# Optimization experiments

Hardware: AMD Instinct MI355X
Metric: run time of the kernel (lower is better)

The kernel has to match this reference:

```python
import jax, jax.numpy as jnp
import numpy as np

B, L, C, R, DK = 8, 2048, 512, 64, 64
H = 2 * C  # hdnSize
NEG = -32767.0  # -2**15 + 1
EPS = 1e-5


def _p(key, shape, std=0.02):
    return (jax.random.normal(key, shape, dtype=jnp.float32) * std)


def setup_inputs() -> dict:
    key = jax.random.key(0)
    ks = jax.random.split(key, 16)
    inp = {
        "x": jax.random.normal(ks[0], (B, L, C), dtype=jnp.float32),
        "maskPAD": jax.random.randint(ks[1], (B, 1, L), 0, 2, dtype=jnp.int32),
        "preScores": jax.random.normal(ks[2], (B, R, R), dtype=jnp.float32),
        "Wp": _p(ks[3], (C, R)), "bp": jnp.zeros((R,), jnp.float32),
        "Wq": _p(ks[4], (C, DK)), "bq": jnp.zeros((DK,), jnp.float32),
        "Wk": _p(ks[5], (C, DK)), "bk": jnp.zeros((DK,), jnp.float32),
        "Wv": _p(ks[6], (C, H)), "bv": jnp.zeros((H,), jnp.float32),
        "Wu": _p(ks[7], (C, H)), "bu": jnp.zeros((H,), jnp.float32),
        "Wo": _p(ks[8], (H, C)), "bo": jnp.zeros((C,), jnp.float32),
        "gamma": jnp.ones((C,), jnp.float32),
        "beta": jnp.zeros((C,), jnp.float32),
    }
    return inp


def reference(x, maskPAD, preScores, Wp, bp, Wq, bq, Wk, bk, Wv, bv, Wu, bu, Wo, bo, gamma, beta):
    # GLU gate: [B,L,H]
    gate = jax.nn.silu(x @ Wu + bu)
    # pseudo-attention logits [B,L,r], masked on padded positions
    pScore = x @ Wp + bp
    pad = (maskPAD[:, 0] == 0)[..., None]  # [B,L,1]
    pScore = jnp.where(pad, NEG, pScore)
    pAlpha = jax.nn.softmax(pScore, axis=1)    # softmax over L (dim=-2)
    pAlpha_ = jax.nn.softmax(pScore, axis=-1)  # softmax over r
    # compress: px [B,r,C]  (== pAlpha.transpose(-1,-2) @ x)
    px = jnp.einsum('blr,blc->brc', pAlpha, x)
    q = jax.nn.silu(px @ Wq + bq)  # [B,r,dk]
    k = jax.nn.silu(px @ Wk + bk)  # [B,r,dk]
    v = jax.nn.silu(px @ Wv + bv)  # [B,r,H]
    scores = jnp.einsum('brd,bsd->brs', q, k) / np.sqrt(DK).astype(np.float32)
    scores = scores + preScores
    alpha = jax.nn.softmax(scores, axis=2)
    z = alpha @ v                                # [B,r,H]
    z = jnp.einsum('blr,brh->blh', pAlpha_, z)   # expand back to [B,L,H]
    z = gate * z
    z = z @ Wo + bo                              # [B,L,C]
    y = x + z
    mu = jnp.mean(y, axis=-1, keepdims=True)
    var = jnp.var(y, axis=-1, keepdims=True)
    out = (y - mu) * jax.lax.rsqrt(var + EPS) * gamma + beta
    return out
```

## Files before the change

### kernel.cpp

```cpp
#include <hip/hip_runtime.h>
#include <hip/hip_bf16.h>

constexpr int B_ = 8;
constexpr int L_ = 2048;
constexpr int C_ = 512;
constexpr int R_ = 64;
constexpr int DK_ = 64;
constexpr int H_ = 1024;
constexpr int M_ = B_ * L_;
constexpr int NQKV_ = 1152;
constexpr float NEG_ = -32767.0f;

__device__ __forceinline__ float toF(float x) { return x; }
__device__ __forceinline__ float toF(__hip_bfloat16 x) { return __bfloat162float(x); }
__device__ __forceinline__ float siluf(float v) { return v / (1.0f + __expf(-v)); }
__device__ __forceinline__ ushort bfbits(float f) {
    __hip_bfloat16 h = __float2bfloat16(f);
    union { __hip_bfloat16 h; ushort u; } cv; cv.h = h; return cv.u;
}
__device__ __forceinline__ float bf2f(ushort u) {
    union { uint u; float f; } cv; cv.u = (uint)u << 16; return cv.f;
}

typedef __attribute__((ext_vector_type(8))) short bf16x8;
// ... 40 lines not shown
    int br1 = n0 + s1 * 16 + sr; if (br1 >= Ndim) br1 = Ndim - 1;
    const ushort* a0p = A  + (size_t)(m0 + s0 * 16 + sr) * Kdim + sc;
    const ushort* a1p = A  + (size_t)(m0 + s1 * 16 + sr) * Kdim + sc;
    const ushort* b0p = Bp + (size_t)br0 * Kdim + sc;
    const ushort* b1p = Bp + (size_t)br1 * Kdim + sc;
    const int lo0 = s0 * 512 + lane * 8;
    const int lo1 = s1 * 512 + lane * 8;

    f32x4 acc[4][4];
#pragma unroll
    for (int a = 0; a < 4; ++a)
#pragma unroll
        for (int b = 0; b < 4; ++b) acc[a][b] = (f32x4){0.f, 0.f, 0.f, 0.f};

    glds16(a0p, &As[0][lo0]);
    glds16(a1p, &As[0][lo1]);
    glds16(b0p, &Bs[0][lo0]);
    glds16(b1p, &Bs[0][lo1]);
    if (32 < Kdim) {
        glds16(a0p + 32, &As[1][lo0]);
        glds16(a1p + 32, &As[1][lo1]);
        glds16(b0p + 32, &Bs[1][lo0]);
        glds16(b1p + 32, &Bs[1][lo1]);
    }

    int cur = 0;
    for (int k0 = 0; k0 < Kdim; k0 += 32) {
        if (k0 + 32 < Kdim) VMCNT(4); else VMCNT(0);
        BARRIER();
        if (k0 + 64 < Kdim) {
            const int nx = cur ? cur - 1 : 2;
            glds16(a0p + k0 + 64, &As[nx][lo0]);
            glds16(a1p + k0 + 64, &As[nx][lo1]);
            glds16(b0p + k0 + 64, &Bs[nx][lo0]);
            glds16(b1p + k0 + 64, &Bs[nx][lo1]);
        }
        bf16x8 af[4], bf[4];
#pragma unroll
        for (int a = 0; a < 4; ++a)
            af[a] = *(const bf16x8*)&As[cur][(wm + a * 16 + lr) * 32 + lq * 8];
#pragma unroll
        for (int b = 0; b < 4; ++b)
            bf[b] = *(const bf16x8*)&Bs[cur][(wn + b * 16 + lr) * 32 + lq * 8];
#pragma unroll
        for (int a = 0; a < 4; ++a)
#pragma unroll
            for (int b = 0; b < 4; ++b)
                acc[a][b] = __builtin_amdgcn_mfma_f32_16x16x32_bf16(af[a], bf[b], acc[a][b], 0, 0, 0);
        cur = (cur == 2) ? 0 : cur + 1;
    }

#pragma unroll
    for (int a = 0; a < 4; ++a) {
#pragma unroll
        for (int b = 0; b < 4; ++b) {
            const int col = n0 + wn + b * 16 + lr;
            if (col < Ndim) {
                const float bn = (EPI == 3) ? 0.f : bias[col];
#pragma unroll
                for (int r = 0; r < 4; ++r) {
                    const int row = m0 + wm + a * 16 + lq * 4 + r;
                    float v = acc[a][b][r];
                    if (EPI == 0) {
                        v = siluf(v + bn);
                        outB[(size_t)row * Ndim + col] = bfbits(v);
                    } else if (EPI == 2) {
                        v += bn + residF[(size_t)row * Ndim + col];
                        outB[(size_t)row * Ndim + col] = bfbits(v);
                    } else {
                        v *= bf2f(residB[(size_t)row * Ndim + col]);
                        outB[(size_t)row * Ndim + col] = bfbits(v);
                    }
                }
            }
        }
    }
}

__global__ __launch_bounds__(256) void pscore_gemm(
    const ushort* __restrict__ x16, const ushort* __restrict__ Wpt,
    const float* __restrict__ bp, const int* __restrict__ mask,
    ushort* __restrict__ pAR16, float* __restrict__ pScoreT)
{
    __shared__ ushort As[3][128 * 32];
    __shared__ ushort Bs[3][64 * 32];

    const int i = blockIdx.x;
    const int G = gridDim.x >> 3;
    const int gi = (i & 7) * G + (i >> 3);
    const int m0 = gi * 128;

    const int tid = threadIdx.x;
    const int lane = tid & 63, w = tid >> 6;
    const int lr = lane & 15, lq = lane >> 4;
    const int sr = lane >> 2, sc = (lane & 3) * 8;
    const int s0 = w * 2, s1 = w * 2 + 1;

    const ushort* a0p = x16 + (size_t)(m0 + s0 * 16 + sr) * C_ + sc;
    const ushort* a1p = x16 + (size_t)(m0 + s1 * 16 + sr) * C_ + sc;
    const ushort* bwp = Wpt + (size_t)(w * 16 + sr) * C_ + sc;
    const int lo0 = s0 * 512 + lane * 8;
    const int lo1 = s1 * 512 + lane * 8;
    const int lob = w * 512 + lane * 8;

    f32x4 acc[2][4];
#pragma unroll
    for (int a = 0; a < 2; ++a)
#pragma unroll
        for (int b = 0; b < 4; ++b) acc[a][b] = (f32x4){0.f, 0.f, 0.f, 0.f};

    glds16(a0p, &As[0][lo0]);
    glds16(a1p, &As[0][lo1]);
    glds16(bwp, &Bs[0][lob]);
    glds16(a0p + 32, &As[1][lo0]);
    glds16(a1p + 32, &As[1][lo1]);
    glds16(bwp + 32, &Bs[1][lob]);

    int cur = 0;
    for (int k0 = 0; k0 < C_; k0 += 32) {
        if (k0 + 32 < C_) VMCNT(3); else VMCNT(0);
        BARRIER();
        if (k0 + 64 < C_) {
            const int nx = cur ? cur - 1 : 2;
            glds16(a0p + k0 + 64, &As[nx][lo0]);
            glds16(a1p + k0 + 64, &As[nx][lo1]);
            glds16(bwp + k0 + 64, &Bs[nx][lob]);
        }
        bf16x8 af[2], bf[4];
#pragma unroll
        for (int a = 0; a < 2; ++a)
            af[a] = *(const bf16x8*)&As[cur][(w * 32 + a * 16 + lr) * 32 + lq * 8];
#pragma unroll
        for (int b = 0; b < 4; ++b)
            bf[b] = *(const bf16x8*)&Bs[cur][(b * 16 + lr) * 32 + lq * 8];
#pragma unroll
        for (int a = 0; a < 2; ++a)
#pragma unroll
            for (int b = 0; b < 4; ++b)
                acc[a][b] = __builtin_amdgcn_mfma_f32_16x16x32_bf16(af[a], bf[b], acc[a][b], 0, 0, 0);
        cur = (cur == 2) ? 0 : cur + 1;
    }

#pragma unroll
    for (int a = 0; a < 2; ++a) {
#pragma unroll
        for (int r = 0; r < 4; ++r) {
            const int row = m0 + w * 32 + a * 16 + lq * 4 + r;
            const bool dead = (mask[row] == 0);
            const int bb = row >> 11, ll = row & (L_ - 1);
            float v[4];
            float mx = -3.4e38f;
#pragma unroll
            for (int b = 0; b < 4; ++b) {
                const int col = b * 16 + lr;
                float t = acc[a][b][r] + bp[col];
                if (dead) t = NEG_;
                v[b] = t;
                pScoreT[((size_t)bb * R_ + col) * L_ + ll] = t;
                mx = fmaxf(mx, t);
            }
#pragma unroll
            for (int o = 1; o < 16; o <<= 1) mx = fmaxf(mx, __shfl_xor(mx, o, 64));
            float e[4], s = 0.f;
#pragma unroll
            for (int b = 0; b < 4; ++b) { e[b] = __expf(v[b] - mx); s += e[b]; }
#pragma unroll
            for (int o = 1; o < 16; o <<= 1) s += __shfl_xor(s, o, 64);
            const float inv = 1.0f / s;
#pragma unroll
            for (int b = 0; b < 4; ++b)
                pAR16[(size_t)row * R_ + b * 16 + lr] = bfbits(e[b] * inv);
        }
    }
}

__global__ __launch_bounds__(256) void fused_gate_z(
    const ushort* __restrict__ x16, const ushort* __restrict__ Wut,
    const float* __restrict__ bu,
    const ushort* __restrict__ pAR, const ushort* __restrict__ zsT,
    ushort* __restrict__ zg)
{
    __shared__ ushort As[3][128 * 32];
    __shared__ ushort Bs[3][128 * 32];

    const int i = blockIdx.x;
    const int G = gridDim.x >> 3;
    const int gi = (i & 7) * G + (i >> 3);
    constexpr int gridN = H_ / 128;
    const int nt = gi % gridN, mt = gi / gridN;
    const int m0 = mt * 128, n0 = nt * 128;

    const int tid = threadIdx.x;
    const int lane = tid & 63, w = tid >> 6;
    const int wm = (w & 1) * 64, wn = (w >> 1) * 64;
    const int lr = lane & 15, lq = lane >> 4;
    const int sr = lane >> 2, sc = (lane & 3) * 8;
    const int s0 = w * 2, s1 = w * 2 + 1;

    const int bidx = m0 >> 11;
    const ushort* a0p = x16 + (size_t)(m0 + s0 * 16 + sr) * C_ + sc;
    const ushort* a1p = x16 + (size_t)(m0 + s1 * 16 + sr) * C_ + sc;
    const ushort* b0p = Wut + (size_t)(n0 + s0 * 16 + sr) * C_ + sc;
    const ushort* b1p = Wut + (size_t)(n0 + s1 * 16 + sr) * C_ + sc;
    const ushort* zb  = zsT + (size_t)bidx * H_ * R_;
    const ushort* c0p = pAR + (size_t)(m0 + s0 * 16 + sr) * R_ + sc;
    const ushort* c1p = pAR + (size_t)(m0 + s1 * 16 + sr) * R_ + sc;
    const ushort* d0p = zb + (size_t)(n0 + s0 * 16 + sr) * R_ + sc;
    const ushort* d1p = zb + (size_t)(n0 + s1 * 16 + sr) * R_ + sc;
    const int lo0 = s0 * 512 + lane * 8;
    const int lo1 = s1 * 512 + lane * 8;

    auto stage = [&](int t, int bsel) {
        if (t < 2) {
            const int off = t * 32;
            glds16(c0p + off, &As[bsel][lo0]);
            glds16(c1p + off, &As[bsel][lo1]);
            glds16(d0p + off, &Bs[bsel][lo0]);
            glds16(d1p + off, &Bs[bsel][lo1]);
        } else {
            const int off = (t - 2) * 32;
            glds16(a0p + off, &As[bsel][lo0]);
            glds16(a1p + off, &As[bsel][lo1]);
            glds16(b0p + off, &Bs[bsel][lo0]);
            glds16(b1p + off, &Bs[bsel][lo1]);
        }
    };

    f32x4 acc[4][4];
#pragma unroll
    for (int a = 0; a < 4; ++a)
#pragma unroll
        for (int b = 0; b < 4; ++b) acc[a][b] = (f32x4){0.f, 0.f, 0.f, 0.f};

    uint pk[4][4][2];

    stage(0, 0);
    stage(1, 1);

    int cur = 0;
    for (int t = 0; t < 18; ++t) {
        if (t < 17) VMCNT(4); else VMCNT(0);
        BARRIER();
        if (t + 2 < 18) stage(t + 2, cur ? cur - 1 : 2);
        bf16x8 af[4], bf[4];
#pragma unroll
        for (int a = 0; a < 4; ++a)
            af[a] = *(const bf16x8*)&As[cur][(wm + a * 16 + lr) * 32 + lq * 8];
#pragma unroll
        for (int b = 0; b < 4; ++b)
            bf[b] = *(const bf16x8*)&Bs[cur][(wn + b * 16 + lr) * 32 + lq * 8];
#pragma unroll
        for (int a = 0; a < 4; ++a)
#pragma unroll
            for (int b = 0; b < 4; ++b)
                acc[a][b] = __builtin_amdgcn_mfma_f32_16x16x32_bf16(af[a], bf[b], acc[a][b], 0, 0, 0);
        if (t == 1) {
#pragma unroll
            for (int a = 0; a < 4; ++a)
#pragma unroll
                for (int b = 0; b < 4; ++b) {
                    pk[a][b][0] = (uint)bfbits(acc[a][b][0]) | ((uint)bfbits(acc[a][b][1]) << 16);
                    pk[a][b][1] = (uint)bfbits(acc[a][b][2]) | ((uint)bfbits(acc[a][b][3]) << 16);
                    acc[a][b] = (f32x4){0.f, 0.f, 0.f, 0.f};
                }
        }
        cur = (cur == 2) ? 0 : cur + 1;
    }

#pragma unroll
    for (int a = 0; a < 4; ++a) {
#pragma unroll
        for (int b = 0; b < 4; ++b) {
            const int col = n0 + wn + b * 16 + lr;
            const float bn = bu[col];
#pragma unroll
            for (int r = 0; r < 4; ++r) {
                const int row = m0 + wm + a * 16 + lq * 4 + r;
                const ushort zu = (ushort)((r & 1) ? (pk[a][b][r >> 1] >> 16)
                                                   : (pk[a][b][r >> 1] & 0xffff));
                const float v = siluf(acc[a][b][r] + bn) * bf2f(zu);
                zg[(size_t)row * H_ + col] = bfbits(v);
            }
        }
    }
}

__global__ __launch_bounds__(256) void x_prep(const float* __restrict__ x,
                                              ushort* __restrict__ x16,
                                              ushort* __restrict__ xT16)
{
    __shared__ float tile[32][33];
    const int tx = threadIdx.x & 31, ty = threadIdx.x >> 5;
    const int c0 = blockIdx.x * 32, l0 = blockIdx.y * 32;
#pragma unroll
    for (int i = 0; i < 32; i += 8) {
        const float v = x[(size_t)(l0 + ty + i) * C_ + c0 + tx];
        tile[ty + i][tx] = v;
        x16[(size_t)(l0 + ty + i) * C_ + c0 + tx] = bfbits(v);
    }
    __syncthreads();
    const int bb = l0 >> 11, ll0 = l0 & (L_ - 1);
#pragma unroll
    for (int i = 0; i < 32; i += 8)
        xT16[((size_t)bb * C_ + c0 + ty + i) * L_ + ll0 + tx] = bfbits(tile[tx][ty + i]);
}

__global__ __launch_bounds__(256) void prep_w(
    const float* __restrict__ Wu, const float* __restrict__ Wo, const float* __restrict__ Wp,
    const float* __restrict__ Wq, const float* __restrict__ bq,
    const float* __restrict__ Wk, const float* __restrict__ bk,
    const float* __restrict__ Wv, const float* __restrict__ bv,
    ushort* __restrict__ Wut, ushort* __restrict__ Wot, ushort* __restrict__ Wpt,
    ushort* __restrict__ Wqkvt, float* __restrict__ bqkv)
{
    int id = blockIdx.x;
    const float* W; ushort* Wt; const float* bsrc = nullptr;
    int K, Nloc, n0, k0, nn0;
    if (id < 512) {
        W = Wu; Wt = Wut; K = 512; Nloc = 1024;
        n0 = (id & 31) * 32; k0 = (id >> 5) * 32; nn0 = n0;
    } else if (id < 1024) {
        id -= 512; W = Wo; Wt = Wot; K = 1024; Nloc = 512;
        n0 = (id & 15) * 32; k0 = (id >> 4) * 32; nn0 = n0;
    } else if (id < 1056) {
        id -= 1024; W = Wp; Wt = Wpt; K = 512; Nloc = 64;
        n0 = (id & 1) * 32; k0 = (id >> 1) * 32; nn0 = n0;
    } else {
        id -= 1056; K = 512; Wt = Wqkvt;
        n0 = (id % 36) * 32; k0 = (id / 36) * 32;
        if (n0 < 64)       { W = Wq; bsrc = bq; Nloc = 64;   nn0 = n0; }
        else if (n0 < 128) { W = Wk; bsrc = bk; Nloc = 64;   nn0 = n0 - 64; }
        else               { W = Wv; bsrc = bv; Nloc = 1024; nn0 = n0 - 128; }
    }
    __shared__ float tile[32][33];
    const int tx = threadIdx.x & 31, ty = threadIdx.x >> 5;
#pragma unroll
    for (int i = 0; i < 32; i += 8)
        tile[ty + i][tx] = W[(size_t)(k0 + ty + i) * Nloc + nn0 + tx];
    __syncthreads();
#pragma unroll
    for (int i = 0; i < 32; i += 8)
        Wt[(size_t)(n0 + ty + i) * K + k0 + tx] = bfbits(tile[tx][ty + i]);
    if (bsrc && k0 == 0 && threadIdx.x < 32) bqkv[n0 + threadIdx.x] = bsrc[nn0 + threadIdx.x];
}

__global__ __launch_bounds__(256) void softmaxL2(const float* __restrict__ pScoreT,
                                                 ushort* __restrict__ pALT)
{
    const size_t br = blockIdx.x;
    const float* row = pScoreT + br * L_;
    ushort* orow = pALT + br * L_;
    const int t = threadIdx.x;
    __shared__ float red[256];

    float v[8];
    float mx = -3.4e38f;
#pragma unroll
    for (int j = 0; j < 8; ++j) { v[j] = row[t + j * 256]; mx = fmaxf(mx, v[j]); }
    red[t] = mx; __syncthreads();
    for (int s = 128; s > 0; s >>= 1) { if (t < s) red[t] = fmaxf(red[t], red[t + s]); __syncthreads(); }
    mx = red[0]; __syncthreads();

    float e[8], sum = 0.f;
#pragma unroll
    for (int j = 0; j < 8; ++j) { e[j] = __expf(v[j] - mx); sum += e[j]; }
    red[t] = sum; __syncthreads();
    for (int s = 128; s > 0; s >>= 1) { if (t < s) red[t] += red[t + s]; __syncthreads(); }
    const float inv = 1.0f / red[0];
#pragma unroll
    for (int j = 0; j < 8; ++j) orow[t + j * 256] = bfbits(e[j] * inv);
}

__global__ __launch_bounds__(512) void compress_mfma(
    const ushort* __restrict__ pALT, const ushort* __restrict__ xT,
    float* __restrict__ parts)
{
    __shared__ ushort As[3][64 * 32];
    __shared__ ushort Bs[3][256 * 32];

    const int bidx = blockIdx.y;
    const int n0 = blockIdx.x * 256;
    const int ks = blockIdx.z;
    const int kbeg = ks * (L_ / 4), kend = kbeg + L_ / 4;
    const int tid = threadIdx.x;
    const int lane = tid & 63, w = tid >> 6;
    const int lr = lane & 15, lq = lane >> 4;
    const int sr = lane >> 2, sc = (lane & 3) * 8;
    const int wm = (w & 1) * 32, wn = (w >> 1) * 64;

    const ushort* Ab = pALT + (size_t)bidx * R_ * L_;
    const ushort* Bb = xT + (size_t)bidx * C_ * L_;

    const int aseg = (w >= 4) ? (w - 4) : 0;
    const ushort* ap = Ab + (size_t)(aseg * 16 + sr) * L_ + sc;
    const int alo = aseg * 512 + lane * 8;
    const ushort* b0p = Bb + (size_t)(n0 + (w * 2) * 16 + sr) * L_ + sc;
    const ushort* b1p = Bb + (size_t)(n0 + (w * 2 + 1) * 16 + sr) * L_ + sc;
    const int blo0 = (w * 2) * 512 + lane * 8;
    const int blo1 = (w * 2 + 1) * 512 + lane * 8;

    auto stage = [&](int k0, int bsel) {
        if (w >= 4) glds16(ap + k0, &As[bsel][alo]);
        glds16(b0p + k0, &Bs[bsel][blo0]);
        glds16(b1p + k0, &Bs[bsel][blo1]);
    };

    f32x4 acc[2][4];
#pragma unroll
    for (int a = 0; a < 2; ++a)
#pragma unroll
        for (int b = 0; b < 4; ++b) acc[a][b] = (f32x4){0.f, 0.f, 0.f, 0.f};

    stage(kbeg, 0);
    stage(kbeg + 32, 1);

    int cur = 0;
    for (int k0 = kbeg; k0 < kend; k0 += 32) {
        if (k0 + 32 < kend) {
            if (w >= 4) VMCNT(3); else VMCNT(2);
        } else {
            VMCNT(0);
        }
        BARRIER();
        if (k0 + 64 < kend) stage(k0 + 64, cur ? cur - 1 : 2);
        bf16x8 af[2], bf[4];
#pragma unroll
        for (int a = 0; a < 2; ++a)
            af[a] = *(const bf16x8*)&As[cur][(wm + a * 16 + lr) * 32 + lq * 8];
#pragma unroll
        for (int b = 0; b < 4; ++b)
            bf[b] = *(const bf16x8*)&Bs[cur][(wn + b * 16 + lr) * 32 + lq * 8];
#pragma unroll
        for (int a = 0; a < 2; ++a)
#pragma unroll
            for (int b = 0; b < 4; ++b)
                acc[a][b] = __builtin_amdgcn_mfma_f32_16x16x32_bf16(af[a], bf[b], acc[a][b], 0, 0, 0);
        cur = (cur == 2) ? 0 : cur + 1;
    }
#pragma unroll
    for (int a = 0; a < 2; ++a)
#pragma unroll
        for (int b = 0; b < 4; ++b)
#pragma unroll
            for (int r = 0; r < 4; ++r) {
                const int row = wm + a * 16 + lq * 4 + r;
                const int col = n0 + wn + b * 16 + lr;
                parts[(((size_t)ks * B_ + bidx) * R_ + row) * C_ + col] = acc[a][b][r];
            }
}

__global__ __launch_bounds__(256) void compress_reduce16(const float* __restrict__ parts,
                                                         ushort* __restrict__ px16)
{
    const size_t i = ((size_t)blockIdx.x * 256 + threadIdx.x) * 4;
    constexpr size_t S = (size_t)B_ * R_ * C_;
    const float4 a = *(const float4*)(parts + i);
    const float4 b = *(const float4*)(parts + i + S);
    const float4 c = *(const float4*)(parts + i + 2 * S);
    const float4 d = *(const float4*)(parts + i + 3 * S);
    ushort4 o;
    o.x = bfbits(a.x + b.x + c.x + d.x);
    o.y = bfbits(a.y + b.y + c.y + d.y);
    o.z = bfbits(a.z + b.z + c.z + d.z);
    o.w = bfbits(a.w + b.w + c.w + d.w);
    *(ushort4*)(px16 + i) = o;
}

__global__ __launch_bounds__(256) void attn_fused(
    const ushort* __restrict__ qkv, const float* __restrict__ preS,
    ushort* __restrict__ zsT)
{
    const int b = blockIdx.x >> 6, r = blockIdx.x & 63;
    const int t = threadIdx.x;
    __shared__ float al[R_];
    if (t < 64) {
        const ushort* qr = qkv + (size_t)(b * R_ + r) * NQKV_;
        const ushort* ks = qkv + (size_t)(b * R_ + t) * NQKV_ + 64;
        float acc = 0.f;
#pragma unroll
        for (int d = 0; d < DK_; d += 4) {
            const ushort4 qa = *(const ushort4*)(qr + d);
            const ushort4 ka = *(const ushort4*)(ks + d);
            acc += bf2f(qa.x) * bf2f(ka.x) + bf2f(qa.y) * bf2f(ka.y)
                 + bf2f(qa.z) * bf2f(ka.z) + bf2f(qa.w) * bf2f(ka.w);
        }
        acc = acc * 0.125f + preS[((size_t)b * R_ + r) * R_ + t];
        float mx = acc;
#pragma unroll
        for (int o = 32; o > 0; o >>= 1) mx = fmaxf(mx, __shfl_xor(mx, o, 64));
        float e = __expf(acc - mx);
        float sm = e;
#pragma unroll
        for (int o = 32; o > 0; o >>= 1) sm += __shfl_xor(sm, o, 64);
        al[t] = e / sm;
    }
    __syncthreads();
    float acc[4] = {};
    for (int s = 0; s < R_; ++s) {
        const float a = al[s];
        const ushort* vr = qkv + (size_t)(b * R_ + s) * NQKV_ + 128;
#pragma unroll
        for (int j = 0; j < 4; ++j) acc[j] += a * bf2f(vr[t + j * 256]);
    }
#pragma unroll
    for (int j = 0; j < 4; ++j) {
        const int h = t + j * 256;
        zsT[((size_t)b * H_ + h) * R_ + r] = bfbits(acc[j]);
    }
}

__global__ __launch_bounds__(256) void layernorm(const __hip_bfloat16* __restrict__ y,
                                                 const float* __restrict__ gamma,
                                                 const float* __restrict__ beta,
                                                 float* __restrict__ out)
{
    const size_t m = blockIdx.x;
    const int t = threadIdx.x;
    const __hip_bfloat16* yr = y + m * C_;
    float v0 = __bfloat162float(yr[t]), v1 = __bfloat162float(yr[t + 256]);
    __shared__ float rs[256], rq[256];
    rs[t] = v0 + v1;
    rq[t] = v0 * v0 + v1 * v1;
    __syncthreads();
    for (int o = 128; o > 0; o >>= 1) {
        if (t < o) { rs[t] += rs[t + o]; rq[t] += rq[t + o]; }
        __syncthreads();
    }
    const float mu = rs[0] * (1.0f / C_);
    const float var = rq[0] * (1.0f / C_) - mu * mu;
    const float inv = rsqrtf(var + 1e-5f);
    out[m * C_ + t] = (v0 - mu) * inv * gamma[t] + beta[t];
    out[m * C_ + t + 256] = (v1 - mu) * inv * gamma[t + 256] + beta[t + 256];
}

template <typename AT, typename BT, typename RT, int ACT, int EPI>
__global__ __launch_bounds__(256) void gemm64(
    const AT* __restrict__ A, const BT* __restrict__ Bw,
    const float* __restrict__ bias, const int* __restrict__ mask,
    const RT* resid, float* __restrict__ outF, __hip_bfloat16* outB,
    int Ndim, int Kdim, long bBatchStride)
{
    __shared__ float As[16][68];
    __shared__ float Bs[16][64];
    const int tid = threadIdx.x;
    const int tx = tid & 15, ty = tid >> 4;
    const int n0 = blockIdx.x * 64, m0 = blockIdx.y * 64;
    const BT* Bp = Bw + (bBatchStride ? (long)(m0 / L_) * bBatchStride : 0);
    float acc[4][4] = {};
    for (int k0 = 0; k0 < Kdim; k0 += 16) {
#pragma unroll
        for (int s = 0; s < 4; ++s) {
            int idx = tid + s * 256;
            int am = idx >> 4, ak = idx & 15;
            As[ak][am] = toF(A[(size_t)(m0 + am) * Kdim + k0 + ak]);
        }
#pragma unroll
        for (int s = 0; s < 4; ++s) {
            int idx = tid + s * 256;
            int bk = idx >> 6, bn = idx & 63;
            Bs[bk][bn] = toF(Bp[(size_t)(k0 + bk) * Ndim + n0 + bn]);
        }
        __syncthreads();
#pragma unroll
        for (int kk = 0; kk < 16; ++kk) {
            float av[4], bv[4];
            *(float4*)av = *(const float4*)&As[kk][ty * 4];
            *(float4*)bv = *(const float4*)&Bs[kk][tx * 4];
#pragma unroll
            for (int i = 0; i < 4; ++i)
#pragma unroll
                for (int j = 0; j < 4; ++j) acc[i][j] += av[i] * bv[j];
        }
        __syncthreads();
    }
#pragma unroll
    for (int i = 0; i < 4; ++i) {
        int m = m0 + ty * 4 + i;
#pragma unroll
        for (int j = 0; j < 4; ++j) {
            int n = n0 + tx * 4 + j;
            float val = acc[i][j];
            if (EPI != 3) val += bias[n];
            if (ACT) val = siluf(val);
            if (EPI == 0) outB[(size_t)m * Ndim + n] = __float2bfloat16(val);
            else if (EPI == 1) { if (mask[m] == 0) val = NEG_; outF[(size_t)m * Ndim + n] = val; }
            else if (EPI == 2) { val += toF(resid[(size_t)m * Ndim + n]); outB[(size_t)m * Ndim + n] = __float2bfloat16(val); }
            else { val *= toF(resid[(size_t)m * Ndim + n]); outB[(size_t)m * Ndim + n] = __float2bfloat16(val); }
        }
    }
}

template <int OUT>
__global__ __launch_bounds__(64) void softmaxR(const float* __restrict__ pScore,
                                               float* __restrict__ outF,
                                               ushort* __restrict__ outU)
{
    const size_t m = blockIdx.x;
    const int t = threadIdx.x;
    float v = pScore[m * R_ + t];
    float mx = v;
#pragma unroll
    for (int o = 32; o > 0; o >>= 1) mx = fmaxf(mx, __shfl_xor(mx, o, 64));
    float e = __expf(v - mx);
    float s = e;
#pragma unroll
    for (int o = 32; o > 0; o >>= 1) s += __shfl_xor(s, o, 64);
    if (OUT == 0) outF[m * R_ + t] = e / s;
    else          outU[m * R_ + t] = bfbits(e / s);
}

__global__ __launch_bounds__(256) void softmaxL(const float* __restrict__ pScore,
                                                float* __restrict__ pAlpha)
{
    const int b = blockIdx.x >> 6, r = blockIdx.x & 63;
    const int t = threadIdx.x;
// ... 142 lines not shown
    float acc[4] = {};
    for (int s = 0; s < R_; ++s) {
        float a = al[s];
        const float* vr = v + ((size_t)b * R_ + s) * H_;
#pragma unroll
        for (int j = 0; j < 4; ++j) acc[j] += a * vr[t + j * 256];
    }
#pragma unroll
    for (int j = 0; j < 4; ++j) {
        const int h = t + j * 256;
        if (MODE == 0) zsF[((size_t)b * R_ + r) * H_ + h] = acc[j];
        else           zsT[((size_t)b * H_ + h) * R_ + r] = bfbits(acc[j]);
    }
}

__global__ __launch_bounds__(64) void attn_scores(
    const float* __restrict__ q, const float* __restrict__ k,
    const float* __restrict__ preS, float* __restrict__ alpha)
{
    const int b = blockIdx.x >> 6, r = blockIdx.x & 63;
    const int s = threadIdx.x;
    const float* qr = q + ((size_t)b * R_ + r) * DK_;
    const float* ks = k + ((size_t)b * R_ + s) * DK_;
    float acc = 0.f;
#pragma unroll
    for (int d = 0; d < DK_; ++d) acc += qr[d] * ks[d];
    acc = acc * 0.125f + preS[((size_t)b * R_ + r) * R_ + s];
    float mx = acc;
#pragma unroll
    for (int o = 32; o > 0; o >>= 1) mx = fmaxf(mx, __shfl_xor(mx, o, 64));
    float e = __expf(acc - mx);
    float sm = e;
#pragma unroll
    for (int o = 32; o > 0; o >>= 1) sm += __shfl_xor(sm, o, 64);
    alpha[((size_t)b * R_ + r) * R_ + s] = e / sm;
}

extern "C" void kernel_launch(void* const* d_in, const int* in_sizes, int n_in,
                              void* d_out, int out_size, void* d_ws, size_t ws_size,
                              hipStream_t stream)
{
    using bf16 = __hip_bfloat16;
    const float* x      = (const float*)d_in[0];
    const int*  maskPAD = (const int*)d_in[1];
    const float* preS   = (const float*)d_in[2];
    const float* Wp     = (const float*)d_in[3];
    const float* bp     = (const float*)d_in[4];
    const float* Wq     = (const float*)d_in[5];
    const float* bq     = (const float*)d_in[6];
    const float* Wk     = (const float*)d_in[7];
    const float* bk     = (const float*)d_in[8];
    const float* Wv     = (const float*)d_in[9];
    const float* bv     = (const float*)d_in[10];
    const float* Wu     = (const float*)d_in[11];
    const float* bu     = (const float*)d_in[12];
    const float* Wo     = (const float*)d_in[13];
    const float* bo     = (const float*)d_in[14];
    const float* gamma  = (const float*)d_in[15];
    const float* beta   = (const float*)d_in[16];
    float* out          = (float*)d_out;

    char* ws = (char*)d_ws;
    const bool bigWS = ws_size >= (size_t)52 * 1024 * 1024;

    if (bigWS) {
        bf16* zg = (bf16*)ws;
        float* parts = (float*)ws;
        char* pool = ws + (size_t)M_ * H_ * 2;
        float* pScoreT = (float*)pool;
        ushort* pALT   = (ushort*)(pScoreT + (size_t)B_ * R_ * L_);
        ushort* pAR16  = pALT + (size_t)B_ * R_ * L_;
        ushort* px16   = pAR16 + (size_t)M_ * R_;
        ushort* qkv16  = px16 + (size_t)B_ * R_ * C_;
        ushort* zsT16  = qkv16 + (size_t)B_ * R_ * NQKV_;
        ushort* Wqkvt  = zsT16 + (size_t)B_ * H_ * R_;
        float*  bqkv   = (float*)(Wqkvt + (size_t)NQKV_ * C_);
        bf16*  y       = (bf16*)pool;
        ushort* Wut    = (ushort*)(pool + 18221568);
        ushort* Wot    = Wut + (size_t)C_ * H_;
        ushort* Wpt    = Wot + (size_t)C_ * H_;
        ushort* x16    = (ushort*)d_out;
        ushort* xT16   = x16 + (size_t)M_ * C_;

        x_prep<<<dim3(C_ / 32, M_ / 32), 256, 0, stream>>>(x, x16, xT16);
        prep_w<<<1632, 256, 0, stream>>>(Wu, Wo, Wp, Wq, bq, Wk, bk, Wv, bv,
                                         Wut, Wot, Wpt, Wqkvt, bqkv);
        pscore_gemm<<<M_ / 128, 256, 0, stream>>>(x16, Wpt, bp, maskPAD, pAR16, pScoreT);
        softmaxL2<<<B_ * R_, 256, 0, stream>>>(pScoreT, pALT);
        compress_mfma<<<dim3(C_ / 256, B_, 4), 512, 0, stream>>>(pALT, xT16, parts);
        compress_reduce16<<<(B_ * R_ * C_) / 1024, 256, 0, stream>>>(parts, px16);
        mfma_gemm5<0><<<(NQKV_ / 128) * ((B_ * R_) / 128), 256, 0, stream>>>(
            px16, Wqkvt, bqkv, nullptr, nullptr, nullptr, qkv16, nullptr, nullptr,
            NQKV_, C_, NQKV_ / 128, 0);
        attn_fused<<<B_ * R_, 256, 0, stream>>>(qkv16, preS, zsT16);
        fused_gate_z<<<(H_ / 128) * (M_ / 128), 256, 0, stream>>>(
            x16, Wut, bu, pAR16, zsT16, (ushort*)zg);
        mfma_gemm5<2><<<(C_ / 128) * (M_ / 128), 256, 0, stream>>>(
            (ushort*)zg, Wot, bo, x, nullptr, nullptr, (ushort*)y, nullptr, nullptr,
            C_, H_, C_ / 128, 0);
        layernorm<<<M_, 256, 0, stream>>>(y, gamma, beta, out);
    } else {
        float* pScore = (float*)ws;
        float* pAL   = pScore + (size_t)M_ * R_;
        float* pAR   = pAL    + (size_t)M_ * R_;
        float* px    = pAR    + (size_t)M_ * R_;
        float* q     = px     + (size_t)B_ * R_ * C_;
        float* kk    = q      + (size_t)B_ * R_ * DK_;
        float* vv    = kk     + (size_t)B_ * R_ * DK_;
        float* alpha = vv     + (size_t)B_ * R_ * H_;
        float* zs    = alpha  + (size_t)B_ * R_ * R_;
        bf16* gate_b = (bf16*)(zs + (size_t)B_ * R_ * H_);
        bf16* y_b    = (bf16*)((char*)gate_b + (size_t)L_ * H_ * 2);

        gemm64<float, float, float, 0, 1><<<dim3(R_ / 64, M_ / 64), 256, 0, stream>>>(
            x, Wp, bp, maskPAD, (const float*)nullptr, pScore, nullptr, R_, C_, 0);
        softmaxL<<<B_ * R_, 256, 0, stream>>>(pScore, pAL);
        softmaxR<0><<<M_, 64, 0, stream>>>(pScore, pAR, nullptr);
        compress_part<<<dim3(C_ / 64, 4, B_), 256, 0, stream>>>(pAL, x, pScore);
        compress_reduce<<<(B_ * R_ * C_) / 256, 256, 0, stream>>>(pScore, px);
        qkv_gemm<<<dim3(2 + H_ / 64, (B_ * R_) / 64), 256, 0, stream>>>(
            px, Wq, bq, Wk, bk, Wv, bv, q, kk, vv);
        attn_scores<<<B_ * R_, 64, 0, stream>>>(q, kk, preS, alpha);
        attn_z<0><<<B_ * R_, 256, 0, stream>>>(alpha, vv, zs, nullptr);

        for (int b = 0; b < B_; ++b) {
            const float* xb = x + (size_t)b * L_ * C_;
            gemm64<float, float, float, 1, 0><<<dim3(H_ / 64, L_ / 64), 256, 0, stream>>>(
                xb, Wu, bu, nullptr, (const float*)nullptr, nullptr, gate_b, H_, C_, 0);
            gemm64<float, float, bf16, 0, 3><<<dim3(H_ / 64, L_ / 64), 256, 0, stream>>>(
                pAR + (size_t)b * L_ * R_, zs + (size_t)b * R_ * H_,
                nullptr, nullptr, gate_b, nullptr, gate_b, H_, R_, 0);
            gemm64<bf16, float, float, 0, 2><<<dim3(C_ / 64, L_ / 64), 256, 0, stream>>>(
                gate_b, Wo, bo, nullptr, xb, nullptr, y_b, C_, H_, 0);
            layernorm<<<L_, 256, 0, stream>>>(y_b, gamma, beta, out + (size_t)b * L_ * C_);
        }
    }
}
```

Baseline: 268.3 us.

## Retile pscore, gate, and compress kernels; merge prep kernels; warp-per-row layernorm

Several unrelated changes. pscore_gemm uses 64-row tiles to double the grid. fused_gate_z moves to 256x128 tiles with 512 threads and double buffering synchronised by __syncthreads. compress_mfma uses 128-wide tiles with an 8-way L split, and its reduce kernel sums 8 partials. The x and weight prep kernels merge into one launch. Layernorm handles one row per wavefront with shuffle reductions and vectorised loads. The aim is to cut launch overhead and raise occupancy and parallelism, at the cost of more partial-sum traffic and a shallower pipeline in the gate GEMM.

```diff
diff --git a/kernel.cpp b/kernel.cpp
--- a/kernel.cpp
+++ b/kernel.cpp
@@ -146,117 +146,101 @@
     const float* __restrict__ bp, const int* __restrict__ mask,
     ushort* __restrict__ pAR16, float* __restrict__ pScoreT)
 {
-    __shared__ ushort As[3][128 * 32];
+    __shared__ ushort As[3][64 * 32];
     __shared__ ushort Bs[3][64 * 32];
 
     const int i = blockIdx.x;
     const int G = gridDim.x >> 3;
     const int gi = (i & 7) * G + (i >> 3);
-    const int m0 = gi * 128;
+    const int m0 = gi * 64;
 
     const int tid = threadIdx.x;
     const int lane = tid & 63, w = tid >> 6;
     const int lr = lane & 15, lq = lane >> 4;
     const int sr = lane >> 2, sc = (lane & 3) * 8;
-    const int s0 = w * 2, s1 = w * 2 + 1;
-
-    const ushort* a0p = x16 + (size_t)(m0 + s0 * 16 + sr) * C_ + sc;
-    const ushort* a1p = x16 + (size_t)(m0 + s1 * 16 + sr) * C_ + sc;
+
+    const ushort* ap  = x16 + (size_t)(m0 + w * 16 + sr) * C_ + sc;
     const ushort* bwp = Wpt + (size_t)(w * 16 + sr) * C_ + sc;
-    const int lo0 = s0 * 512 + lane * 8;
-    const int lo1 = s1 * 512 + lane * 8;
-    const int lob = w * 512 + lane * 8;
-
-    f32x4 acc[2][4];
-#pragma unroll
-    for (int a = 0; a < 2; ++a)
-#pragma unroll
-        for (int b = 0; b < 4; ++b) acc[a][b] = (f32x4){0.f, 0.f, 0.f, 0.f};
-
-    glds16(a0p, &As[0][lo0]);
-    glds16(a1p, &As[0][lo1]);
-    glds16(bwp, &Bs[0][lob]);
-    glds16(a0p + 32, &As[1][lo0]);
-    glds16(a1p + 32, &As[1][lo1]);
-    glds16(bwp + 32, &Bs[1][lob]);
+    const int loa = w * 512 + lane * 8;
+
+    f32x4 acc[4];
+#pragma unroll
+    for (int b = 0; b < 4; ++b) acc[b] = (f32x4){0.f, 0.f, 0.f, 0.f};
+
+    glds16(ap, &As[0][loa]);
+    glds16(bwp, &Bs[0][loa]);
+    glds16(ap + 32, &As[1][loa]);
+    glds16(bwp + 32, &Bs[1][loa]);
 
     int cur = 0;
     for (int k0 = 0; k0 < C_; k0 += 32) {
-        if (k0 + 32 < C_) VMCNT(3); else VMCNT(0);
+        if (k0 + 32 < C_) VMCNT(2); else VMCNT(0);
         BARRIER();
         if (k0 + 64 < C_) {
             const int nx = cur ? cur - 1 : 2;
-            glds16(a0p + k0 + 64, &As[nx][lo0]);
-            glds16(a1p + k0 + 64, &As[nx][lo1]);
-            glds16(bwp + k0 + 64, &Bs[nx][lob]);
-        }
-        bf16x8 af[2], bf[4];
-#pragma unroll
-        for (int a = 0; a < 2; ++a)
-            af[a] = *(const bf16x8*)&As[cur][(w * 32 + a * 16 + lr) * 32 + lq * 8];
+            glds16(ap + k0 + 64, &As[nx][loa]);
+            glds16(bwp + k0 + 64, &Bs[nx][loa]);
+        }
+        bf16x8 af, bf[4];
+        af = *(const bf16x8*)&As[cur][(w * 16 + lr) * 32 + lq * 8];
 #pragma unroll
         for (int b = 0; b < 4; ++b)
             bf[b] = *(const bf16x8*)&Bs[cur][(b * 16 + lr) * 32 + lq * 8];
 #pragma unroll
-        for (int a = 0; a < 2; ++a)
-#pragma unroll
-            for (int b = 0; b < 4; ++b)
-                acc[a][b] = __builtin_amdgcn_mfma_f32_16x16x32_bf16(af[a], bf[b], acc[a][b], 0, 0, 0);
+        for (int b = 0; b < 4; ++b)
+            acc[b] = __builtin_amdgcn_mfma_f32_16x16x32_bf16(af, bf[b], acc[b], 0, 0, 0);
         cur = (cur == 2) ? 0 : cur + 1;
     }
 
 #pragma unroll
-    for (int a = 0; a < 2; ++a) {
-#pragma unroll
-        for (int r = 0; r < 4; ++r) {
-            const int row = m0 + w * 32 + a * 16 + lq * 4 + r;
-            const bool dead = (mask[row] == 0);
-            const int bb = row >> 11, ll = row & (L_ - 1);
-            float v[4];
-            float mx = -3.4e38f;
-#pragma unroll
-            for (int b = 0; b < 4; ++b) {
-                const int col = b * 16 + lr;
-                float t = acc[a][b][r] + bp[col];
-                if (dead) t = NEG_;
-                v[b] = t;
-                pScoreT[((size_t)bb * R_ + col) * L_ + ll] = t;
-                mx = fmaxf(mx, t);
-            }
-#pragma unroll
-            for (int o = 1; o < 16; o <<= 1) mx = fmaxf(mx, __shfl_xor(mx, o, 64));
-            float e[4], s = 0.f;
-#pragma unroll
-            for (int b = 0; b < 4; ++b) { e[b] = __expf(v[b] - mx); s += e[b]; }
-#pragma unroll
-            for (int o = 1; o < 16; o <<= 1) s += __shfl_xor(s, o, 64);
-            const float inv = 1.0f / s;
-#pragma unroll
-            for (int b = 0; b < 4; ++b)
-                pAR16[(size_t)row * R_ + b * 16 + lr] = bfbits(e[b] * inv);
-        }
-    }
-}
-
-__global__ __launch_bounds__(256) void fused_gate_z(
+    for (int r = 0; r < 4; ++r) {
+        const int row = m0 + w * 16 + lq * 4 + r;
+        const bool dead = (mask[row] == 0);
+        const int bb = row >> 11, ll = row & (L_ - 1);
+        float v[4];
+        float mx = -3.4e38f;
+#pragma unroll
+        for (int b = 0; b < 4; ++b) {
+            const int col = b * 16 + lr;
+            float t = acc[b][r] + bp[col];
+            if (dead) t = NEG_;
+            v[b] = t;
+            pScoreT[((size_t)bb * R_ + col) * L_ + ll] = t;
+            mx = fmaxf(mx, t);
+        }
+#pragma unroll
+        for (int o = 1; o < 16; o <<= 1) mx = fmaxf(mx, __shfl_xor(mx, o, 64));
+        float e[4], s = 0.f;
+#pragma unroll
+        for (int b = 0; b < 4; ++b) { e[b] = __expf(v[b] - mx); s += e[b]; }
+#pragma unroll
+        for (int o = 1; o < 16; o <<= 1) s += __shfl_xor(s, o, 64);
+        const float inv = 1.0f / s;
+#pragma unroll
+        for (int b = 0; b < 4; ++b)
+            pAR16[(size_t)row * R_ + b * 16 + lr] = bfbits(e[b] * inv);
+    }
+}
+
+__global__ __launch_bounds__(512) void fused_gate_z(
     const ushort* __restrict__ x16, const ushort* __restrict__ Wut,
     const float* __restrict__ bu,
     const ushort* __restrict__ pAR, const ushort* __restrict__ zsT,
     ushort* __restrict__ zg)
 {
-    __shared__ ushort As[3][128 * 32];
-    __shared__ ushort Bs[3][128 * 32];
+    __shared__ ushort As[2][256 * 32];
+    __shared__ ushort Bs[2][128 * 32];
 
     const int i = blockIdx.x;
     const int G = gridDim.x >> 3;
     const int gi = (i & 7) * G + (i >> 3);
     constexpr int gridN = H_ / 128;
     const int nt = gi % gridN, mt = gi / gridN;
-    const int m0 = mt * 128, n0 = nt * 128;
+    const int m0 = mt * 256, n0 = nt * 128;
 
     const int tid = threadIdx.x;
     const int lane = tid & 63, w = tid >> 6;
-    const int wm = (w & 1) * 64, wn = (w >> 1) * 64;
+    const int wm = (w & 3) * 64, wn = (w >> 2) * 64;
     const int lr = lane & 15, lq = lane >> 4;
     const int sr = lane >> 2, sc = (lane & 3) * 8;
     const int s0 = w * 2, s1 = w * 2 + 1;
@@ -264,29 +248,26 @@
     const int bidx = m0 >> 11;
     const ushort* a0p = x16 + (size_t)(m0 + s0 * 16 + sr) * C_ + sc;
     const ushort* a1p = x16 + (size_t)(m0 + s1 * 16 + sr) * C_ + sc;
-    const ushort* b0p = Wut + (size_t)(n0 + s0 * 16 + sr) * C_ + sc;
-    const ushort* b1p = Wut + (size_t)(n0 + s1 * 16 + sr) * C_ + sc;
+    const ushort* b0p = Wut + (size_t)(n0 + w * 16 + sr) * C_ + sc;
     const ushort* zb  = zsT + (size_t)bidx * H_ * R_;
     const ushort* c0p = pAR + (size_t)(m0 + s0 * 16 + sr) * R_ + sc;
     const ushort* c1p = pAR + (size_t)(m0 + s1 * 16 + sr) * R_ + sc;
-    const ushort* d0p = zb + (size_t)(n0 + s0 * 16 + sr) * R_ + sc;
-    const ushort* d1p = zb + (size_t)(n0 + s1 * 16 + sr) * R_ + sc;
+    const ushort* d0p = zb + (size_t)(n0 + w * 16 + sr) * R_ + sc;
     const int lo0 = s0 * 512 + lane * 8;
     const int lo1 = s1 * 512 + lane * 8;
+    const int lob = w * 512 + lane * 8;
 
     auto stage = [&](int t, int bsel) {
         if (t < 2) {
             const int off = t * 32;
             glds16(c0p + off, &As[bsel][lo0]);
             glds16(c1p + off, &As[bsel][lo1]);
-            glds16(d0p + off, &Bs[bsel][lo0]);
-            glds16(d1p + off, &Bs[bsel][lo1]);
+            glds16(d0p + off, &Bs[bsel][lob]);
         } else {
             const int off = (t - 2) * 32;
             glds16(a0p + off, &As[bsel][lo0]);
             glds16(a1p + off, &As[bsel][lo1]);
-            glds16(b0p + off, &Bs[bsel][lo0]);
-            glds16(b1p + off, &Bs[bsel][lo1]);
+            glds16(b0p + off, &Bs[bsel][lob]);
         }
     };
 
@@ -299,13 +280,11 @@
     uint pk[4][4][2];
 
     stage(0, 0);
-    stage(1, 1);
 
     int cur = 0;
     for (int t = 0; t < 18; ++t) {
-        if (t < 17) VMCNT(4); else VMCNT(0);
-        BARRIER();
-        if (t + 2 < 18) stage(t + 2, cur ? cur - 1 : 2);
+        __syncthreads();
+        if (t + 1 < 18) stage(t + 1, cur ^ 1);
         bf16x8 af[4], bf[4];
 #pragma unroll
         for (int a = 0; a < 4; ++a)
@@ -328,7 +307,7 @@
                     acc[a][b] = (f32x4){0.f, 0.f, 0.f, 0.f};
                 }
         }
-        cur = (cur == 2) ? 0 : cur + 1;
+        cur ^= 1;
     }
 
 #pragma unroll
@@ -349,27 +328,8 @@
     }
 }
 
-__global__ __launch_bounds__(256) void x_prep(const float* __restrict__ x,
-                                              ushort* __restrict__ x16,
-                                              ushort* __restrict__ xT16)
-{
-    __shared__ float tile[32][33];
-    const int tx = threadIdx.x & 31, ty = threadIdx.x >> 5;
-    const int c0 = blockIdx.x * 32, l0 = blockIdx.y * 32;
-#pragma unroll
-    for (int i = 0; i < 32; i += 8) {
-        const float v = x[(size_t)(l0 + ty + i) * C_ + c0 + tx];
-        tile[ty + i][tx] = v;
-        x16[(size_t)(l0 + ty + i) * C_ + c0 + tx] = bfbits(v);
-    }
-    __syncthreads();
-    const int bb = l0 >> 11, ll0 = l0 & (L_ - 1);
-#pragma unroll
-    for (int i = 0; i < 32; i += 8)
-        xT16[((size_t)bb * C_ + c0 + ty + i) * L_ + ll0 + tx] = bfbits(tile[tx][ty + i]);
-}
-
-__global__ __launch_bounds__(256) void prep_w(
+__global__ __launch_bounds__(256) void xw_prep(
+    const float* __restrict__ x, ushort* __restrict__ x16, ushort* __restrict__ xT16,
     const float* __restrict__ Wu, const float* __restrict__ Wo, const float* __restrict__ Wp,
     const float* __restrict__ Wq, const float* __restrict__ bq,
     const float* __restrict__ Wk, const float* __restrict__ bk,
@@ -377,7 +337,27 @@
     ushort* __restrict__ Wut, ushort* __restrict__ Wot, ushort* __restrict__ Wpt,
     ushort* __restrict__ Wqkvt, float* __restrict__ bqkv)
 {
+    __shared__ float tile[32][33];
+    const int tx = threadIdx.x & 31, ty = threadIdx.x >> 5;
     int id = blockIdx.x;
+
+    if (id < 8192) {
+        const int c0 = (id & 15) * 32, l0 = (id >> 4) * 32;
+#pragma unroll
+        for (int i = 0; i < 32; i += 8) {
+            const float v = x[(size_t)(l0 + ty + i) * C_ + c0 + tx];
+            tile[ty + i][tx] = v;
+            x16[(size_t)(l0 + ty + i) * C_ + c0 + tx] = bfbits(v);
+        }
+        __syncthreads();
+        const int bb = l0 >> 11, ll0 = l0 & (L_ - 1);
+#pragma unroll
+        for (int i = 0; i < 32; i += 8)
+            xT16[((size_t)bb * C_ + c0 + ty + i) * L_ + ll0 + tx] = bfbits(tile[tx][ty + i]);
+        return;
+    }
+    id -= 8192;
+
     const float* W; ushort* Wt; const float* bsrc = nullptr;
     int K, Nloc, n0, k0, nn0;
     if (id < 512) {
@@ -396,8 +376,6 @@
         else if (n0 < 128) { W = Wk; bsrc = bk; Nloc = 64;   nn0 = n0 - 64; }
         else               { W = Wv; bsrc = bv; Nloc = 1024; nn0 = n0 - 128; }
     }
-    __shared__ float tile[32][33];
-    const int tx = threadIdx.x & 31, ty = threadIdx.x >> 5;
 #pragma unroll
     for (int i = 0; i < 32; i += 8)
         tile[ty + i][tx] = W[(size_t)(k0 + ty + i) * Nloc + nn0 + tx];
@@ -435,17 +413,17 @@
     for (int j = 0; j < 8; ++j) orow[t + j * 256] = bfbits(e[j] * inv);
 }
 
-__global__ __launch_bounds__(512) void compress_mfma(
+__global__ __launch_bounds__(256) void compress_mfma(
     const ushort* __restrict__ pALT, const ushort* __restrict__ xT,
     float* __restrict__ parts)
 {
     __shared__ ushort As[3][64 * 32];
-    __shared__ ushort Bs[3][256 * 32];
+    __shared__ ushort Bs[3][128 * 32];
 
     const int bidx = blockIdx.y;
-    const int n0 = blockIdx.x * 256;
+    const int n0 = blockIdx.x * 128;
     const int ks = blockIdx.z;
-    const int kbeg = ks * (L_ / 4), kend = kbeg + L_ / 4;
+    const int kbeg = ks * (L_ / 8), kend = kbeg + L_ / 8;
     const int tid = threadIdx.x;
     const int lane = tid & 63, w = tid >> 6;
     const int lr = lane & 15, lq = lane >> 4;
@@ -455,16 +433,15 @@
     const ushort* Ab = pALT + (size_t)bidx * R_ * L_;
     const ushort* Bb = xT + (size_t)bidx * C_ * L_;
 
-    const int aseg = (w >= 4) ? (w - 4) : 0;
-    const ushort* ap = Ab + (size_t)(aseg * 16 + sr) * L_ + sc;
-    const int alo = aseg * 512 + lane * 8;
-    const ushort* b0p = Bb + (size_t)(n0 + (w * 2) * 16 + sr) * L_ + sc;
-    const ushort* b1p = Bb + (size_t)(n0 + (w * 2 + 1) * 16 + sr) * L_ + sc;
-    const int blo0 = (w * 2) * 512 + lane * 8;
-    const int blo1 = (w * 2 + 1) * 512 + lane * 8;
+    const ushort* ap  = Ab + (size_t)(w * 16 + sr) * L_ + sc;
+    const ushort* b0p = Bb + (size_t)(n0 + (2 * w) * 16 + sr) * L_ + sc;
+    const ushort* b1p = Bb + (size_t)(n0 + (2 * w + 1) * 16 + sr) * L_ + sc;
+    const int alo  = w * 512 + lane * 8;
+    const int blo0 = (2 * w) * 512 + lane * 8;
+    const int blo1 = (2 * w + 1) * 512 + lane * 8;
 
     auto stage = [&](int k0, int bsel) {
-        if (w >= 4) glds16(ap + k0, &As[bsel][alo]);
+        glds16(ap + k0, &As[bsel][alo]);
         glds16(b0p + k0, &Bs[bsel][blo0]);
         glds16(b1p + k0, &Bs[bsel][blo1]);
     };
@@ -480,11 +457,7 @@
 
     int cur = 0;
     for (int k0 = kbeg; k0 < kend; k0 += 32) {
-        if (k0 + 32 < kend) {
-            if (w >= 4) VMCNT(3); else VMCNT(2);
-        } else {
-            VMCNT(0);
-        }
+        if (k0 + 32 < kend) VMCNT(3); else VMCNT(0);
         BARRIER();
         if (k0 + 64 < kend) stage(k0 + 64, cur ? cur - 1 : 2);
         bf16x8 af[2], bf[4];
@@ -518,15 +491,14 @@
 {
     const size_t i = ((size_t)blockIdx.x * 256 + threadIdx.x) * 4;
     constexpr size_t S = (size_t)B_ * R_ * C_;
-    const float4 a = *(const float4*)(parts + i);
-    const float4 b = *(const float4*)(parts + i + S);
-    const float4 c = *(const float4*)(parts + i + 2 * S);
-    const float4 d = *(const float4*)(parts + i + 3 * S);
+    float4 s = *(const float4*)(parts + i);
+#pragma unroll
+    for (int k = 1; k < 8; ++k) {
+        const float4 p = *(const float4*)(parts + i + (size_t)k * S);
+        s.x += p.x; s.y += p.y; s.z += p.z; s.w += p.w;
+    }
     ushort4 o;
-    o.x = bfbits(a.x + b.x + c.x + d.x);
-    o.y = bfbits(a.y + b.y + c.y + d.y);
-    o.z = bfbits(a.z + b.z + c.z + d.z);
-    o.w = bfbits(a.w + b.w + c.w + d.w);
+    o.x = bfbits(s.x); o.y = bfbits(s.y); o.z = bfbits(s.z); o.w = bfbits(s.w);
     *(ushort4*)(px16 + i) = o;
 }
 
@@ -573,28 +545,44 @@
     }
 }
 
-__global__ __launch_bounds__(256) void layernorm(const __hip_bfloat16* __restrict__ y,
+__global__ __launch_bounds__(256) void layernorm(const ushort* __restrict__ y,
                                                  const float* __restrict__ gamma,
                                                  const float* __restrict__ beta,
                                                  float* __restrict__ out)
 {
-    const size_t m = blockIdx.x;
-    const int t = threadIdx.x;
-    const __hip_bfloat16* yr = y + m * C_;
-    float v0 = __bfloat162float(yr[t]), v1 = __bfloat162float(yr[t + 256]);
-    __shared__ float rs[256], rq[256];
-    rs[t] = v0 + v1;
-    rq[t] = v0 * v0 + v1 * v1;
-    __syncthreads();
-    for (int o = 128; o > 0; o >>= 1) {
-        if (t < o) { rs[t] += rs[t + o]; rq[t] += rq[t + o]; }
-        __syncthreads();
-    }
-    const float mu = rs[0] * (1.0f / C_);
-    const float var = rq[0] * (1.0f / C_) - mu * mu;
+    const int w = threadIdx.x >> 6, lane = threadIdx.x & 63;
+    const size_t m = (size_t)blockIdx.x * 4 + w;
+    const ushort* yr = y + m * C_ + lane * 8;
+    const ushort4 p0 = *(const ushort4*)(yr);
+    const ushort4 p1 = *(const ushort4*)(yr + 4);
+    float v[8] = { bf2f(p0.x), bf2f(p0.y), bf2f(p0.z), bf2f(p0.w),
+                   bf2f(p1.x), bf2f(p1.y), bf2f(p1.z), bf2f(p1.w) };
+    float s = 0.f, q = 0.f;
+#pragma unroll
+    for (int j = 0; j < 8; ++j) { s += v[j]; q += v[j] * v[j]; }
+#pragma unroll
+    for (int o = 32; o > 0; o >>= 1) {
+        s += __shfl_xor(s, o, 64);
+        q += __shfl_xor(q, o, 64);
+    }
+    const float mu = s * (1.0f / C_);
+    const float var = q * (1.0f / C_) - mu * mu;
     const float inv = rsqrtf(var + 1e-5f);
-    out[m * C_ + t] = (v0 - mu) * inv * gamma[t] + beta[t];
-    out[m * C_ + t + 256] = (v1 - mu) * inv * gamma[t + 256] + beta[t + 256];
+    const float4 g0 = *(const float4*)(gamma + lane * 8);
+    const float4 g1 = *(const float4*)(gamma + lane * 8 + 4);
+    const float4 b0 = *(const float4*)(beta + lane * 8);
+    const float4 b1 = *(const float4*)(beta + lane * 8 + 4);
+    float4 o0, o1;
+    o0.x = (v[0] - mu) * inv * g0.x + b0.x;
+    o0.y = (v[1] - mu) * inv * g0.y + b0.y;
+    o0.z = (v[2] - mu) * inv * g0.z + b0.z;
+    o0.w = (v[3] - mu) * inv * g0.w + b0.w;
+    o1.x = (v[4] - mu) * inv * g1.x + b1.x;
+    o1.y = (v[5] - mu) * inv * g1.y + b1.y;
+    o1.z = (v[6] - mu) * inv * g1.z + b1.z;
+    o1.w = (v[7] - mu) * inv * g1.w + b1.w;
+    *(float4*)(out + m * C_ + lane * 8) = o0;
+    *(float4*)(out + m * C_ + lane * 8 + 4) = o1;
 }
 
 template <typename AT, typename BT, typename RT, int ACT, int EPI>
@@ -903,23 +891,23 @@
         ushort* x16    = (ushort*)d_out;
         ushort* xT16   = x16 + (size_t)M_ * C_;
 
-        x_prep<<<dim3(C_ / 32, M_ / 32), 256, 0, stream>>>(x, x16, xT16);
-        prep_w<<<1632, 256, 0, stream>>>(Wu, Wo, Wp, Wq, bq, Wk, bk, Wv, bv,
-                                         Wut, Wot, Wpt, Wqkvt, bqkv);
-        pscore_gemm<<<M_ / 128, 256, 0, stream>>>(x16, Wpt, bp, maskPAD, pAR16, pScoreT);
+        xw_prep<<<8192 + 1632, 256, 0, stream>>>(
+            x, x16, xT16, Wu, Wo, Wp, Wq, bq, Wk, bk, Wv, bv,
+            Wut, Wot, Wpt, Wqkvt, bqkv);
+        pscore_gemm<<<M_ / 64, 256, 0, stream>>>(x16, Wpt, bp, maskPAD, pAR16, pScoreT);
         softmaxL2<<<B_ * R_, 256, 0, stream>>>(pScoreT, pALT);
-        compress_mfma<<<dim3(C_ / 256, B_, 4), 512, 0, stream>>>(pALT, xT16, parts);
+        compress_mfma<<<dim3(C_ / 128, B_, 8), 256, 0, stream>>>(pALT, xT16, parts);
         compress_reduce16<<<(B_ * R_ * C_) / 1024, 256, 0, stream>>>(parts, px16);
         mfma_gemm5<0><<<(NQKV_ / 128) * ((B_ * R_) / 128), 256, 0, stream>>>(
             px16, Wqkvt, bqkv, nullptr, nullptr, nullptr, qkv16, nullptr, nullptr,
             NQKV_, C_, NQKV_ / 128, 0);
         attn_fused<<<B_ * R_, 256, 0, stream>>>(qkv16, preS, zsT16);
-        fused_gate_z<<<(H_ / 128) * (M_ / 128), 256, 0, stream>>>(
+        fused_gate_z<<<(H_ / 128) * (M_ / 256), 512, 0, stream>>>(
             x16, Wut, bu, pAR16, zsT16, (ushort*)zg);
         mfma_gemm5<2><<<(C_ / 128) * (M_ / 128), 256, 0, stream>>>(
             (ushort*)zg, Wot, bo, x, nullptr, nullptr, (ushort*)y, nullptr, nullptr,
             C_, H_, C_ / 128, 0);
-        layernorm<<<M_, 256, 0, stream>>>(y, gamma, beta, out);
+        layernorm<<<M_ / 4, 256, 0, stream>>>((const ushort*)y, gamma, beta, out);
     } else {
         float* pScore = (float*)ws;
         float* pAL   = pScore + (size_t)M_ * R_;
@@ -953,7 +941,7 @@
                 nullptr, nullptr, gate_b, nullptr, gate_b, H_, R_, 0);
             gemm64<bf16, float, float, 0, 2><<<dim3(C_ / 64, L_ / 64), 256, 0, stream>>>(
                 gate_b, Wo, bo, nullptr, xb, nullptr, y_b, C_, H_, 0);
-            layernorm<<<L_, 256, 0, stream>>>(y_b, gamma, beta, out + (size_t)b * L_ * C_);
-        }
-    }
-}
+            layernorm<<<L_ / 4, 256, 0, stream>>>((const ushort*)y_b, gamma, beta, out + (size_t)b * L_ * C_);
+        }
+    }
+}
```

Result: faster. 256.4 us (-4.4%).
